# Optimization experiments

Measured on AMD Instinct MI355X. Metric: run time of the kernel, lower is better.

Reference implementation:

```python
import jax, jax.numpy as jnp
import numpy as np

B, S, H, DK = 2, 2048, 16, 64
D = H * DK  # d_model = 1024


def setup_inputs() -> dict:
    key = jax.random.key(0)
    ks = jax.random.split(key, 12)
    inp = {
        "queries": jax.random.normal(ks[0], (B, S, D), jnp.float32),
        "keys": jax.random.normal(ks[1], (B, S, D), jnp.float32),
        "values": jax.random.normal(ks[2], (B, S, D), jnp.float32),
        # additive 0/1 mask (1 = masked out), causal upper-triangular
        "mask": jnp.triu(jnp.ones((S, S), jnp.float32), k=1)[None, None, :, :],
        "W_q": jax.random.normal(ks[3], (D, D), jnp.float32) / np.sqrt(D),
        "b_q": jnp.zeros((D,), jnp.float32),
        "W_k": jax.random.normal(ks[4], (D, D), jnp.float32) / np.sqrt(D),
        "b_k": jnp.zeros((D,), jnp.float32),
        "W_v": jax.random.normal(ks[5], (D, D), jnp.float32) / np.sqrt(D),
        "b_v": jnp.zeros((D,), jnp.float32),
        "W_o": jax.random.normal(ks[6], (D, D), jnp.float32) / np.sqrt(D),
        "b_o": jnp.zeros((D,), jnp.float32),
    }
    return inp


def _split_heads(x):
    # (B, S, D) -> (B, H, S, DK)
    return x.reshape(x.shape[0], x.shape[1], H, DK).transpose(0, 2, 1, 3)


def reference(queries, keys, values, mask, W_q, b_q, W_k, b_k, W_v, b_v, W_o, b_o):
    q = _split_heads(queries @ W_q + b_q)  # (B, H, S, DK)
    k = _split_heads(keys @ W_k + b_k)
    v = _split_heads(values @ W_v + b_v)
    scale = 1.0 / jnp.sqrt(jnp.asarray(DK, q.dtype))
    scores = jnp.einsum("bhqd,bhkd->bhqk", q, k) * scale  # (B, H, S, S)
    scores = scores + (-1e9) * mask
    weights = jax.nn.softmax(scores, axis=-1)
    o = jnp.einsum("bhqk,bhkd->bhqd", weights, v)  # (B, H, S, DK)
    o = o.transpose(0, 2, 1, 3).reshape(queries.shape[0], queries.shape[1], D)
    return o @ W_o + b_o
```

## Files before the change

### kernel.cpp

```cpp
#include <hip/hip_runtime.h>
#include <hip/hip_bf16.h>
#include <stdint.h>

typedef unsigned short u16;
typedef __attribute__((ext_vector_type(4))) float f32x4;
typedef __attribute__((ext_vector_type(8))) short bf16x8;
typedef __attribute__((ext_vector_type(4))) short s16x4;

#define B_ 2
#define S_ 2048
#define H_ 16
#define D_ 1024
#define XELEMS (B_*S_*D_)
#define WELEMS (D_*D_)

__device__ __forceinline__ u16 f2bf(float f) {
  union { float f; unsigned u; } v; v.f = f;
  unsigned r = v.u + 0x7fffu + ((v.u >> 16) & 1u);
  return (u16)(r >> 16);
}

__device__ __forceinline__ void async16(const void* g, void* l) {
  __builtin_amdgcn_global_load_lds(
      (const __attribute__((address_space(1))) unsigned int*)g,
      (__attribute__((address_space(3))) unsigned int*)l, 16, 0, 0);
}

#if __has_builtin(__builtin_amdgcn_exp2f)
#define EXP2(x) __builtin_amdgcn_exp2f(x)
#else
#define EXP2(x) exp2f(x)
#endif

__device__ __forceinline__ unsigned cvtpk(float a, float b) {
  unsigned r;
  asm("v_cvt_pk_bf16_f32 %0, %1, %2" : "=v"(r) : "v"(a), "v"(b));
  return r;
}

__global__ __launch_bounds__(256) void prep_k(
    const float* __restrict__ q, const float* __restrict__ k,
    const float* __restrict__ v,
    const float* __restrict__ Wq, const float* __restrict__ Wk,
    const float* __restrict__ Wv, const float* __restrict__ Wo,
    u16* __restrict__ X, u16* __restrict__ WT) {
  const int bid = blockIdx.x;
  if (bid < 4096) {
    __shared__ float tile[32][33];
    const int z = bid >> 10, rem = bid & 1023;
    const float* W = (z == 0) ? Wq : (z == 1) ? Wk : (z == 2) ? Wv : Wo;
    u16* o = WT + z * WELEMS;
    const int r0 = (rem >> 5) << 5, c0 = (rem & 31) << 5;
    const int tx = threadIdx.x & 31, ty = threadIdx.x >> 5;
    #pragma unroll
    for (int rr = ty; rr < 32; rr += 8)
      tile[rr][tx] = W[(r0 + rr) * D_ + c0 + tx];
    __syncthreads();
    #pragma unroll
    for (int rr = ty; rr < 32; rr += 8)
      o[(c0 + rr) * D_ + r0 + tx] = f2bf(tile[tx][rr]);
  } else {
    const int cb = bid - 4096;
    const int ngrp = XELEMS / 8;
    const int total = 3 * ngrp;
    for (int i = cb * 256 + threadIdx.x; i < total; i += 1024 * 256) {
      int which = i / ngrp;
      int off = (i - which * ngrp) * 8;
      const float* src = (which == 0) ? q : (which == 1) ? k : v;
      float4 a = *(const float4*)(src + off);
      float4 b = *(const float4*)(src + off + 4);
      u16 rr[8] = {f2bf(a.x), f2bf(a.y), f2bf(a.z), f2bf(a.w),
                   f2bf(b.x), f2bf(b.y), f2bf(b.z), f2bf(b.w)};
      uint4 pk;
      pk.x = (unsigned)rr[0] | ((unsigned)rr[1] << 16);
      pk.y = (unsigned)rr[2] | ((unsigned)rr[3] << 16);
      pk.z = (unsigned)rr[4] | ((unsigned)rr[5] << 16);
      pk.w = (unsigned)rr[6] | ((unsigned)rr[7] << 16);
      *(uint4*)(X + which * XELEMS + off) = pk;
    }
  }
}

template <int MODE>
__device__ __forceinline__ void gemm_body(const u16* __restrict__ A,
                                          const u16* __restrict__ BT,
                                          const float* __restrict__ bias,
                                          void* __restrict__ outp,
                                          int bm, int bn) {
  __shared__ __align__(16) u16 As[128 * 64];
  __shared__ __align__(16) u16 Bs[128 * 64];
  const int tid = threadIdx.x;
  const int w = tid >> 6, l = tid & 63;
  const int wr = w >> 1, wc = w & 1;
  const int g = l >> 4, r = l & 15;
  (void)w; (void)l;

  f32x4 acc[4][4];
  #pragma unroll
  for (int i = 0; i < 4; i++)
    #pragma unroll
    for (int j = 0; j < 4; j++) acc[i][j] = (f32x4){0.f, 0.f, 0.f, 0.f};

  int dst[4], aoff[4], boff[4];
  #pragma unroll
  for (int i = 0; i < 4; i++) {
    const int o = i * 4096 + tid * 16;
    dst[i] = o;
    const int row = o >> 7;
    const int cbyte = (o & 127) ^ ((row & 7) << 4);
    aoff[i] = (bm + row) * 1024 + (cbyte >> 1);
    boff[i] = (bn + row) * 1024 + (cbyte >> 1);
  }

  for (int k0 = 0; k0 < 1024; k0 += 64) {
    #pragma unroll
    for (int i = 0; i < 4; i++) async16(A + aoff[i] + k0, (char*)As + dst[i]);
    #pragma unroll
    for (int i = 0; i < 4; i++) async16(BT + boff[i] + k0, (char*)Bs + dst[i]);
    __syncthreads();
    bf16x8 af[2][4], bf[2][4];
    #pragma unroll
    for (int kk = 0; kk < 2; kk++)
      #pragma unroll
      for (int mi = 0; mi < 4; mi++) {
        const int rA = wr * 64 + mi * 16 + r;
        af[kk][mi] = *(const bf16x8*)((const char*)As +
            ((rA * 128 + kk * 64 + g * 16) ^ ((rA & 7) << 4)));
      }
    #pragma unroll
    for (int kk = 0; kk < 2; kk++)
      #pragma unroll
      for (int ni = 0; ni < 4; ni++) {
        const int rB = wc * 64 + ni * 16 + r;
        bf[kk][ni] = *(const bf16x8*)((const char*)Bs +
            ((rB * 128 + kk * 64 + g * 16) ^ ((rB & 7) << 4)));
      }
    #pragma unroll
    for (int kk = 0; kk < 2; kk++)
      #pragma unroll
      for (int mi = 0; mi < 4; mi++)
        #pragma unroll
        for (int ni = 0; ni < 4; ni++)
          acc[mi][ni] = __builtin_amdgcn_mfma_f32_16x16x32_bf16(
              af[kk][mi], bf[kk][ni], acc[mi][ni], 0, 0, 0);
    __syncthreads();
  }

  const int col0 = bn + wc * 64;
  float bc[4];
  #pragma unroll
  for (int ni = 0; ni < 4; ni++) bc[ni] = bias[col0 + ni * 16 + r];

  if (MODE == 0) {
    u16* out = (u16*)outp;
    #pragma unroll
    for (int mi = 0; mi < 4; mi++) {
      const int row = bm + wr * 64 + mi * 16 + g * 4;
      #pragma unroll
      for (int ni = 0; ni < 4; ni++) {
        const int col = col0 + ni * 16 + r;
        const int h = col >> 6, dk = col & 63;
        #pragma unroll
        for (int i = 0; i < 4; i++) {
          const int rr = row + i;
          const int b = rr >> 11, s = rr & 2047;
          out[(((b << 4) | h) * 2048 + s) * 64 + dk] =
              f2bf(acc[mi][ni][i] + bc[ni]);
        }
      }
    }
  } else if (MODE == 2) {
    u16* out = (u16*)outp;
    #pragma unroll
    for (int mi = 0; mi < 4; mi++) {
      const int row = bm + wr * 64 + mi * 16 + g * 4;
      #pragma unroll
      for (int ni = 0; ni < 4; ni++) {
        const int col = col0 + ni * 16 + r;
        const int h = col >> 6, dk = col & 63;
        #pragma unroll
        for (int i = 0; i < 4; i++) {
          const int rr = row + i;
          const int b = rr >> 11, s = rr & 2047;
          out[((((b << 4) | h) * 64 + dk) * 2048) + s] =
              f2bf(acc[mi][ni][i] + bc[ni]);
        }
      }
    }
  } else {
    float* out = (float*)outp;
    #pragma unroll
    for (int mi = 0; mi < 4; mi++) {
      const int row = bm + wr * 64 + mi * 16 + g * 4;
      #pragma unroll
      for (int ni = 0; ni < 4; ni++) {
        const int col = col0 + ni * 16 + r;
        #pragma unroll
        for (int i = 0; i < 4; i++)
          out[(row + i) * 1024 + col] = acc[mi][ni][i] + bc[ni];
      }
    }
  }
}

__global__ __launch_bounds__(256) void gemm_qkv_k(
    const u16* __restrict__ X, const u16* __restrict__ WT,
    const float* __restrict__ bq, const float* __restrict__ bk,
    const float* __restrict__ bv, u16* __restrict__ QKV) {
  const int z = blockIdx.z;
  const float* bias = (z == 0) ? bq : (z == 1) ? bk : bv;
  if (z == 2)
    gemm_body<2>(X + z * XELEMS, WT + z * WELEMS, bias, QKV + z * XELEMS,
                 blockIdx.x * 128, blockIdx.y * 128);
  else
    gemm_body<0>(X + z * XELEMS, WT + z * WELEMS, bias, QKV + z * XELEMS,
                 blockIdx.x * 128, blockIdx.y * 128);
}

__global__ __launch_bounds__(256) void gemm_o_k(
    const u16* __restrict__ O, const u16* __restrict__ WOT,
    const float* __restrict__ bo, float* __restrict__ out) {
  gemm_body<1>(O, WOT, bo, out, blockIdx.x * 128, blockIdx.y * 128);
}

__global__ __launch_bounds__(256) void attn_k(
    const u16* __restrict__ Qh, const u16* __restrict__ Kh,
    const u16* __restrict__ VTh, u16* __restrict__ O) {
  __shared__ __align__(16) char ldsK[2][8192];
  __shared__ __align__(16) char ldsV[2][8192];
  __shared__ __align__(16) u16 ldsP[4][16 * 72];

  const int bh = blockIdx.y;
  const int pj = blockIdx.x;
  const int tid = threadIdx.x;
  const int w = tid >> 6, l = tid & 63;
  const int g = l >> 4, r = l & 15;
  const int b = bh >> 4, h = bh & 15;

  const u16* Qp = Qh + bh * (S_ * 64);
  const char* Kp = (const char*)(Kh + bh * (S_ * 64));
  const char* Vp = (const char*)(VTh + bh * (64 * S_));

  int kdst[2], ksrc[2], vfix[2];
  #pragma unroll
  for (int i = 0; i < 2; i++) {
    const int o = (w * 2 + i) * 1024 + l * 16;
    kdst[i] = o;
    ksrc[i] = o ^ (((o >> 7) & 7) << 4);
    const int d = o >> 7, cbyte = o & 127;
    vfix[i] = d * (S_ * 2) + (cbyte ^ ((d & 7) << 4));
  }
  u16* Pq = &ldsP[w][0];

  #pragma unroll
  for (int pass = 0; pass < 2; pass++) {
    const int qt = pass ? (31 - pj) : pj;
    const int q0w = qt * 64 + w * 16;
    const int nt = qt + 1;
    const int qloc = w * 16 + r;

    bf16x8 qf[2];
    #pragma unroll
    for (int dh = 0; dh < 2; dh++)
      qf[dh] = *(const bf16x8*)(Qp + (q0w + r) * 64 + dh * 32 + g * 8);
    asm volatile("s_waitcnt vmcnt(0)" ::: "memory");

    f32x4 accT[4];
    #pragma unroll
    for (int dn = 0; dn < 4; dn++) accT[dn] = (f32x4){0.f, 0.f, 0.f, 0.f};
    float mrun = -1e30f, lsum = 0.f;

    #pragma unroll
    for (int i = 0; i < 2; i++) {
      async16(Kp + ksrc[i], &ldsK[0][0] + kdst[i]);
      async16(Vp + vfix[i], &ldsV[0][0] + kdst[i]);
    }

    for (int t = 0; t < nt; ++t) {
      const int buf = t & 1;
      if (t + 1 < nt) {
        const char* Ks = Kp + (t + 1) * 8192;
        const char* Vs = Vp + (t + 1) * 128;
        #pragma unroll
        for (int i = 0; i < 2; i++) {
          async16(Ks + ksrc[i], &ldsK[buf ^ 1][0] + kdst[i]);
          async16(Vs + vfix[i], &ldsV[buf ^ 1][0] + kdst[i]);
        }
        asm volatile("s_waitcnt vmcnt(4)" ::: "memory");
      } else {
        asm volatile("s_waitcnt vmcnt(0)" ::: "memory");
      }
      asm volatile("s_barrier" ::: "memory");

      const char* Kb = &ldsK[buf][0];
      f32x4 sc[4];
      #pragma unroll
      for (int ct = 0; ct < 4; ct++) {
        const int row = ct * 16 + r;
        const int sw = (row & 7) << 4;
        bf16x8 k0 = *(const bf16x8*)(Kb + ((row * 128 + g * 16) ^ sw));
        bf16x8 k1 = *(const bf16x8*)(Kb + ((row * 128 + 64 + g * 16) ^ sw));
        f32x4 z = (f32x4){0.f, 0.f, 0.f, 0.f};
        z = __builtin_amdgcn_mfma_f32_16x16x32_bf16(k0, qf[0], z, 0, 0, 0);
        sc[ct] = __builtin_amdgcn_mfma_f32_16x16x32_bf16(k1, qf[1], z, 0, 0, 0);
      }

      const bool diag = (t == nt - 1);
      #pragma unroll
      for (int ct = 0; ct < 4; ct++)
        #pragma unroll
        for (int i = 0; i < 4; i++) {
          float s = sc[ct][i] * 0.18033688f;
          if (diag && (ct * 16 + g * 4 + i > qloc)) s = -1e9f;
          sc[ct][i] = s;
        }

      float a0 = fmaxf(fmaxf(sc[0][0], sc[0][1]), sc[0][2]);
      float a1 = fmaxf(fmaxf(sc[0][3], sc[1][0]), sc[1][1]);
      float a2 = fmaxf(fmaxf(sc[1][2], sc[1][3]), sc[2][0]);
      float a3 = fmaxf(fmaxf(sc[2][1], sc[2][2]), sc[2][3]);
      float a4 = fmaxf(fmaxf(sc[3][0], sc[3][1]), sc[3][2]);
      float pmax = fmaxf(fmaxf(fmaxf(a0, a1), fmaxf(a2, a3)),
                         fmaxf(a4, sc[3][3]));
      pmax = fmaxf(pmax, __shfl_xor(pmax, 16, 64));
      pmax = fmaxf(pmax, __shfl_xor(pmax, 32, 64));

      if (!__all(pmax - mrun <= 11.0f)) {
        const float mnew = fmaxf(mrun, pmax);
        const float corr = EXP2(mrun - mnew);
        mrun = mnew;
        #pragma unroll
        for (int dn = 0; dn < 4; dn++)
          #pragma unroll
          for (int i = 0; i < 4; i++) accT[dn][i] *= corr;
        lsum *= corr;
      }

      float ps = 0.f;
      #pragma unroll
      for (int ct = 0; ct < 4; ct++)
        #pragma unroll
        for (int i = 0; i < 4; i++) {
          const float p = EXP2(sc[ct][i] - mrun);
          sc[ct][i] = p;
          ps += p;
        }
      ps += __shfl_xor(ps, 16, 64);
      ps += __shfl_xor(ps, 32, 64);
      lsum += ps;

      #pragma unroll
      for (int ct = 0; ct < 4; ct++) {
        uint2 pk;
        pk.x = cvtpk(sc[ct][0], sc[ct][1]);
        pk.y = cvtpk(sc[ct][2], sc[ct][3]);
        *(uint2*)&Pq[r * 72 + ct * 16 + g * 4] = pk;
      }
      asm volatile("s_waitcnt lgkmcnt(0)" ::: "memory");

      const char* Vb = &ldsV[buf][0];
      bf16x8 pf[2];
      #pragma unroll
      for (int kp = 0; kp < 2; kp++)
        pf[kp] = *(const bf16x8*)&Pq[r * 72 + kp * 32 + g * 8];
      __builtin_amdgcn_s_setprio(1);
      #pragma unroll
      for (int dn = 0; dn < 4; dn++) {
        const int vrow = dn * 16 + r;
        const int vsw = (vrow & 7) << 4;
        #pragma unroll
        for (int kp = 0; kp < 2; kp++) {
          bf16x8 vf = *(const bf16x8*)(Vb + ((vrow * 128 + kp * 64 + g * 16) ^ vsw));
          accT[dn] = __builtin_amdgcn_mfma_f32_16x16x32_bf16(vf, pf[kp], accT[dn], 0, 0, 0);
        }
      }
      __builtin_amdgcn_s_setprio(0);
      asm volatile("s_barrier" ::: "memory");
    }

    const float inv = 1.0f / lsum;
    const int qrow = q0w + r;
    #pragma unroll
    for (int dn = 0; dn < 4; dn++) {
      u16 o0 = f2bf(accT[dn][0] * inv), o1 = f2bf(accT[dn][1] * inv);
      u16 o2 = f2bf(accT[dn][2] * inv), o3 = f2bf(accT[dn][3] * inv);
      uint2 pk;
      pk.x = (unsigned)o0 | ((unsigned)o1 << 16);
      pk.y = (unsigned)o2 | ((unsigned)o3 << 16);
      *(uint2*)(O + ((size_t)(b * 2048 + qrow)) * 1024 + h * 64 + dn * 16 + g * 4) = pk;
    }
  }
}

extern "C" void kernel_launch(void* const* d_in, const int* in_sizes, int n_in,
                              void* d_out, int out_size, void* d_ws, size_t ws_size,
                              hipStream_t stream) {
  const float* q  = (const float*)d_in[0];
  const float* k  = (const float*)d_in[1];
  const float* v  = (const float*)d_in[2];
  const float* Wq = (const float*)d_in[4];
  const float* bq = (const float*)d_in[5];
  const float* Wk = (const float*)d_in[6];
  const float* bk = (const float*)d_in[7];
  const float* Wv = (const float*)d_in[8];
  const float* bv = (const float*)d_in[9];
  const float* Wo = (const float*)d_in[10];
  const float* bo = (const float*)d_in[11];

  char* ws = (char*)d_ws;
  const size_t MB = 1u << 20;
  u16* X   = (u16*)(ws);
  u16* WT  = (u16*)(ws + 24 * MB);
  u16* QKV = (u16*)(ws + 32 * MB);
  u16* O   = (u16*)(ws);

  hipLaunchKernelGGL(prep_k, dim3(5120), dim3(256), 0, stream,
                     q, k, v, Wq, Wk, Wv, Wo, X, WT);
  hipLaunchKernelGGL(gemm_qkv_k, dim3(32, 8, 3), dim3(256), 0, stream,
                     X, WT, bq, bk, bv, QKV);
  hipLaunchKernelGGL(attn_k, dim3(16, 32), dim3(256), 0, stream,
                     QKV, QKV + XELEMS, QKV + 2 * XELEMS, O);
  hipLaunchKernelGGL(gemm_o_k, dim3(32, 8), dim3(256), 0, stream,
                     O, WT + 3 * WELEMS, bo, (float*)d_out);
}
```

Measured before the change: 137.3 us.

## Double-buffer GEMM K-loop with async prefetch and split attention into per-tile blocks

The GEMM main loop now uses two LDS buffers, issuing the async global-to-LDS loads for the next K slice before computing the current one. It waits with vmcnt and raw barriers instead of __syncthreads, and raises wave priority around the MFMA block. The attention kernel drops its paired two-pass scheme, in which each block handled q-tiles pj and 31-pj. It now launches one block per q-tile (32x32 grid), heaviest tiles first, to add parallelism and rely on the scheduler for balance. This doubles GEMM LDS use, which may lower occupancy, and makes attention blocks uneven in work.

```diff
diff --git a/kernel.cpp b/kernel.cpp
--- a/kernel.cpp
+++ b/kernel.cpp
@@ -87,8 +87,8 @@
                                           const float* __restrict__ bias,
                                           void* __restrict__ outp,
                                           int bm, int bn) {
-  __shared__ __align__(16) u16 As[128 * 64];
-  __shared__ __align__(16) u16 Bs[128 * 64];
+  __shared__ __align__(16) u16 As[2][128 * 64];
+  __shared__ __align__(16) u16 Bs[2][128 * 64];
   const int tid = threadIdx.x;
   const int w = tid >> 6, l = tid & 63;
   const int wr = w >> 1, wc = w & 1;
@@ -112,19 +112,34 @@
     boff[i] = (bn + row) * 1024 + (cbyte >> 1);
   }
 
-  for (int k0 = 0; k0 < 1024; k0 += 64) {
-    #pragma unroll
-    for (int i = 0; i < 4; i++) async16(A + aoff[i] + k0, (char*)As + dst[i]);
-    #pragma unroll
-    for (int i = 0; i < 4; i++) async16(BT + boff[i] + k0, (char*)Bs + dst[i]);
-    __syncthreads();
+  #pragma unroll
+  for (int i = 0; i < 4; i++) {
+    async16(A + aoff[i], (char*)As[0] + dst[i]);
+    async16(BT + boff[i], (char*)Bs[0] + dst[i]);
+  }
+
+  for (int t = 0; t < 16; ++t) {
+    const int buf = t & 1;
+    if (t < 15) {
+      const int k0 = (t + 1) * 64;
+      #pragma unroll
+      for (int i = 0; i < 4; i++) {
+        async16(A + aoff[i] + k0, (char*)As[buf ^ 1] + dst[i]);
+        async16(BT + boff[i] + k0, (char*)Bs[buf ^ 1] + dst[i]);
+      }
+      asm volatile("s_waitcnt vmcnt(8)" ::: "memory");
+    } else {
+      asm volatile("s_waitcnt vmcnt(0)" ::: "memory");
+    }
+    asm volatile("s_barrier" ::: "memory");
+
     bf16x8 af[2][4], bf[2][4];
     #pragma unroll
     for (int kk = 0; kk < 2; kk++)
       #pragma unroll
       for (int mi = 0; mi < 4; mi++) {
         const int rA = wr * 64 + mi * 16 + r;
-        af[kk][mi] = *(const bf16x8*)((const char*)As +
+        af[kk][mi] = *(const bf16x8*)((const char*)As[buf] +
             ((rA * 128 + kk * 64 + g * 16) ^ ((rA & 7) << 4)));
       }
     #pragma unroll
@@ -132,9 +147,10 @@
       #pragma unroll
       for (int ni = 0; ni < 4; ni++) {
         const int rB = wc * 64 + ni * 16 + r;
-        bf[kk][ni] = *(const bf16x8*)((const char*)Bs +
+        bf[kk][ni] = *(const bf16x8*)((const char*)Bs[buf] +
             ((rB * 128 + kk * 64 + g * 16) ^ ((rB & 7) << 4)));
       }
+    __builtin_amdgcn_s_setprio(1);
     #pragma unroll
     for (int kk = 0; kk < 2; kk++)
       #pragma unroll
@@ -143,7 +159,8 @@
         for (int ni = 0; ni < 4; ni++)
           acc[mi][ni] = __builtin_amdgcn_mfma_f32_16x16x32_bf16(
               af[kk][mi], bf[kk][ni], acc[mi][ni], 0, 0, 0);
-    __syncthreads();
+    __builtin_amdgcn_s_setprio(0);
+    asm volatile("s_barrier" ::: "memory");
   }
 
   const int col0 = bn + wc * 64;
@@ -231,7 +248,7 @@
   __shared__ __align__(16) u16 ldsP[4][16 * 72];
 
   const int bh = blockIdx.y;
-  const int pj = blockIdx.x;
+  const int qt = 31 - blockIdx.x;
   const int tid = threadIdx.x;
   const int w = tid >> 6, l = tid & 63;
   const int g = l >> 4, r = l & 15;
@@ -252,143 +269,139 @@
   }
   u16* Pq = &ldsP[w][0];
 
-  #pragma unroll
-  for (int pass = 0; pass < 2; pass++) {
-    const int qt = pass ? (31 - pj) : pj;
-    const int q0w = qt * 64 + w * 16;
-    const int nt = qt + 1;
-    const int qloc = w * 16 + r;
-
-    bf16x8 qf[2];
-    #pragma unroll
-    for (int dh = 0; dh < 2; dh++)
-      qf[dh] = *(const bf16x8*)(Qp + (q0w + r) * 64 + dh * 32 + g * 8);
-    asm volatile("s_waitcnt vmcnt(0)" ::: "memory");
-
-    f32x4 accT[4];
-    #pragma unroll
-    for (int dn = 0; dn < 4; dn++) accT[dn] = (f32x4){0.f, 0.f, 0.f, 0.f};
-    float mrun = -1e30f, lsum = 0.f;
-
-    #pragma unroll
-    for (int i = 0; i < 2; i++) {
-      async16(Kp + ksrc[i], &ldsK[0][0] + kdst[i]);
-      async16(Vp + vfix[i], &ldsV[0][0] + kdst[i]);
-    }
-
-    for (int t = 0; t < nt; ++t) {
-      const int buf = t & 1;
-      if (t + 1 < nt) {
-        const char* Ks = Kp + (t + 1) * 8192;
-        const char* Vs = Vp + (t + 1) * 128;
+  const int q0w = qt * 64 + w * 16;
+  const int nt = qt + 1;
+  const int qloc = w * 16 + r;
+
+  bf16x8 qf[2];
+  #pragma unroll
+  for (int dh = 0; dh < 2; dh++)
+    qf[dh] = *(const bf16x8*)(Qp + (q0w + r) * 64 + dh * 32 + g * 8);
+  asm volatile("s_waitcnt vmcnt(0)" ::: "memory");
+
+  f32x4 accT[4];
+  #pragma unroll
+  for (int dn = 0; dn < 4; dn++) accT[dn] = (f32x4){0.f, 0.f, 0.f, 0.f};
+  float mrun = -1e30f, lsum = 0.f;
+
+  #pragma unroll
+  for (int i = 0; i < 2; i++) {
+    async16(Kp + ksrc[i], &ldsK[0][0] + kdst[i]);
+    async16(Vp + vfix[i], &ldsV[0][0] + kdst[i]);
+  }
+
+  for (int t = 0; t < nt; ++t) {
+    const int buf = t & 1;
+    if (t + 1 < nt) {
+      const char* Ks = Kp + (t + 1) * 8192;
+      const char* Vs = Vp + (t + 1) * 128;
+      #pragma unroll
+      for (int i = 0; i < 2; i++) {
+        async16(Ks + ksrc[i], &ldsK[buf ^ 1][0] + kdst[i]);
+        async16(Vs + vfix[i], &ldsV[buf ^ 1][0] + kdst[i]);
+      }
+      asm volatile("s_waitcnt vmcnt(4)" ::: "memory");
+    } else {
+      asm volatile("s_waitcnt vmcnt(0)" ::: "memory");
+    }
+    asm volatile("s_barrier" ::: "memory");
+
+    const char* Kb = &ldsK[buf][0];
+    f32x4 sc[4];
+    #pragma unroll
+    for (int ct = 0; ct < 4; ct++) {
+      const int row = ct * 16 + r;
+      const int sw = (row & 7) << 4;
+      bf16x8 k0 = *(const bf16x8*)(Kb + ((row * 128 + g * 16) ^ sw));
+      bf16x8 k1 = *(const bf16x8*)(Kb + ((row * 128 + 64 + g * 16) ^ sw));
+      f32x4 z = (f32x4){0.f, 0.f, 0.f, 0.f};
+      z = __builtin_amdgcn_mfma_f32_16x16x32_bf16(k0, qf[0], z, 0, 0, 0);
+      sc[ct] = __builtin_amdgcn_mfma_f32_16x16x32_bf16(k1, qf[1], z, 0, 0, 0);
+    }
+
+    const bool diag = (t == nt - 1);
+    #pragma unroll
+    for (int ct = 0; ct < 4; ct++)
+      #pragma unroll
+      for (int i = 0; i < 4; i++) {
+        float s = sc[ct][i] * 0.18033688f;
+        if (diag && (ct * 16 + g * 4 + i > qloc)) s = -1e9f;
+        sc[ct][i] = s;
+      }
+
+    float a0 = fmaxf(fmaxf(sc[0][0], sc[0][1]), sc[0][2]);
+    float a1 = fmaxf(fmaxf(sc[0][3], sc[1][0]), sc[1][1]);
+    float a2 = fmaxf(fmaxf(sc[1][2], sc[1][3]), sc[2][0]);
+    float a3 = fmaxf(fmaxf(sc[2][1], sc[2][2]), sc[2][3]);
+    float a4 = fmaxf(fmaxf(sc[3][0], sc[3][1]), sc[3][2]);
+    float pmax = fmaxf(fmaxf(fmaxf(a0, a1), fmaxf(a2, a3)),
+                       fmaxf(a4, sc[3][3]));
+    pmax = fmaxf(pmax, __shfl_xor(pmax, 16, 64));
+    pmax = fmaxf(pmax, __shfl_xor(pmax, 32, 64));
+
+    if (!__all(pmax - mrun <= 11.0f)) {
+      const float mnew = fmaxf(mrun, pmax);
+      const float corr = EXP2(mrun - mnew);
+      mrun = mnew;
+      #pragma unroll
+      for (int dn = 0; dn < 4; dn++)
         #pragma unroll
-        for (int i = 0; i < 2; i++) {
-          async16(Ks + ksrc[i], &ldsK[buf ^ 1][0] + kdst[i]);
-          async16(Vs + vfix[i], &ldsV[buf ^ 1][0] + kdst[i]);
-        }
-        asm volatile("s_waitcnt vmcnt(4)" ::: "memory");
-      } else {
-        asm volatile("s_waitcnt vmcnt(0)" ::: "memory");
-      }
-      asm volatile("s_barrier" ::: "memory");
-
-      const char* Kb = &ldsK[buf][0];
-      f32x4 sc[4];
-      #pragma unroll
-      for (int ct = 0; ct < 4; ct++) {
-        const int row = ct * 16 + r;
-        const int sw = (row & 7) << 4;
-        bf16x8 k0 = *(const bf16x8*)(Kb + ((row * 128 + g * 16) ^ sw));
-        bf16x8 k1 = *(const bf16x8*)(Kb + ((row * 128 + 64 + g * 16) ^ sw));
-        f32x4 z = (f32x4){0.f, 0.f, 0.f, 0.f};
-        z = __builtin_amdgcn_mfma_f32_16x16x32_bf16(k0, qf[0], z, 0, 0, 0);
-        sc[ct] = __builtin_amdgcn_mfma_f32_16x16x32_bf16(k1, qf[1], z, 0, 0, 0);
-      }
-
-      const bool diag = (t == nt - 1);
-      #pragma unroll
-      for (int ct = 0; ct < 4; ct++)
-        #pragma unroll
-        for (int i = 0; i < 4; i++) {
-          float s = sc[ct][i] * 0.18033688f;
-          if (diag && (ct * 16 + g * 4 + i > qloc)) s = -1e9f;
-          sc[ct][i] = s;
-        }
-
-      float a0 = fmaxf(fmaxf(sc[0][0], sc[0][1]), sc[0][2]);
-      float a1 = fmaxf(fmaxf(sc[0][3], sc[1][0]), sc[1][1]);
-      float a2 = fmaxf(fmaxf(sc[1][2], sc[1][3]), sc[2][0]);
-      float a3 = fmaxf(fmaxf(sc[2][1], sc[2][2]), sc[2][3]);
-      float a4 = fmaxf(fmaxf(sc[3][0], sc[3][1]), sc[3][2]);
-      float pmax = fmaxf(fmaxf(fmaxf(a0, a1), fmaxf(a2, a3)),
-                         fmaxf(a4, sc[3][3]));
-      pmax = fmaxf(pmax, __shfl_xor(pmax, 16, 64));
-      pmax = fmaxf(pmax, __shfl_xor(pmax, 32, 64));
-
-      if (!__all(pmax - mrun <= 11.0f)) {
-        const float mnew = fmaxf(mrun, pmax);
-        const float corr = EXP2(mrun - mnew);
-        mrun = mnew;
-        #pragma unroll
-        for (int dn = 0; dn < 4; dn++)
-          #pragma unroll
-          for (int i = 0; i < 4; i++) accT[dn][i] *= corr;
-        lsum *= corr;
-      }
-
-      float ps = 0.f;
-      #pragma unroll
-      for (int ct = 0; ct < 4; ct++)
-        #pragma unroll
-        for (int i = 0; i < 4; i++) {
-          const float p = EXP2(sc[ct][i] - mrun);
-          sc[ct][i] = p;
-          ps += p;
-        }
-      ps += __shfl_xor(ps, 16, 64);
-      ps += __shfl_xor(ps, 32, 64);
-      lsum += ps;
-
-      #pragma unroll
-      for (int ct = 0; ct < 4; ct++) {
-        uint2 pk;
-        pk.x = cvtpk(sc[ct][0], sc[ct][1]);
-        pk.y = cvtpk(sc[ct][2], sc[ct][3]);
-        *(uint2*)&Pq[r * 72 + ct * 16 + g * 4] = pk;
-      }
-      asm volatile("s_waitcnt lgkmcnt(0)" ::: "memory");
-
-      const char* Vb = &ldsV[buf][0];
-      bf16x8 pf[2];
-      #pragma unroll
-      for (int kp = 0; kp < 2; kp++)
-        pf[kp] = *(const bf16x8*)&Pq[r * 72 + kp * 32 + g * 8];
-      __builtin_amdgcn_s_setprio(1);
-      #pragma unroll
-      for (int dn = 0; dn < 4; dn++) {
-        const int vrow = dn * 16 + r;
-        const int vsw = (vrow & 7) << 4;
-        #pragma unroll
-        for (int kp = 0; kp < 2; kp++) {
-          bf16x8 vf = *(const bf16x8*)(Vb + ((vrow * 128 + kp * 64 + g * 16) ^ vsw));
-          accT[dn] = __builtin_amdgcn_mfma_f32_16x16x32_bf16(vf, pf[kp], accT[dn], 0, 0, 0);
-        }
-      }
-      __builtin_amdgcn_s_setprio(0);
-      asm volatile("s_barrier" ::: "memory");
-    }
-
-    const float inv = 1.0f / lsum;
-    const int qrow = q0w + r;
+        for (int i = 0; i < 4; i++) accT[dn][i] *= corr;
+      lsum *= corr;
+    }
+
+    float ps = 0.f;
+    #pragma unroll
+    for (int ct = 0; ct < 4; ct++)
+      #pragma unroll
+      for (int i = 0; i < 4; i++) {
+        const float p = EXP2(sc[ct][i] - mrun);
+        sc[ct][i] = p;
+        ps += p;
+      }
+    ps += __shfl_xor(ps, 16, 64);
+    ps += __shfl_xor(ps, 32, 64);
+    lsum += ps;
+
+    #pragma unroll
+    for (int ct = 0; ct < 4; ct++) {
+      uint2 pk;
+      pk.x = cvtpk(sc[ct][0], sc[ct][1]);
+      pk.y = cvtpk(sc[ct][2], sc[ct][3]);
+      *(uint2*)&Pq[r * 72 + ct * 16 + g * 4] = pk;
+    }
+    asm volatile("s_waitcnt lgkmcnt(0)" ::: "memory");
+
+    const char* Vb = &ldsV[buf][0];
+    bf16x8 pf[2];
+    #pragma unroll
+    for (int kp = 0; kp < 2; kp++)
+      pf[kp] = *(const bf16x8*)&Pq[r * 72 + kp * 32 + g * 8];
+    __builtin_amdgcn_s_setprio(1);
     #pragma unroll
     for (int dn = 0; dn < 4; dn++) {
-      u16 o0 = f2bf(accT[dn][0] * inv), o1 = f2bf(accT[dn][1] * inv);
-      u16 o2 = f2bf(accT[dn][2] * inv), o3 = f2bf(accT[dn][3] * inv);
-      uint2 pk;
-      pk.x = (unsigned)o0 | ((unsigned)o1 << 16);
-      pk.y = (unsigned)o2 | ((unsigned)o3 << 16);
-      *(uint2*)(O + ((size_t)(b * 2048 + qrow)) * 1024 + h * 64 + dn * 16 + g * 4) = pk;
-    }
+      const int vrow = dn * 16 + r;
+      const int vsw = (vrow & 7) << 4;
+      #pragma unroll
+      for (int kp = 0; kp < 2; kp++) {
+        bf16x8 vf = *(const bf16x8*)(Vb + ((vrow * 128 + kp * 64 + g * 16) ^ vsw));
+        accT[dn] = __builtin_amdgcn_mfma_f32_16x16x32_bf16(vf, pf[kp], accT[dn], 0, 0, 0);
+      }
+    }
+    __builtin_amdgcn_s_setprio(0);
+    asm volatile("s_barrier" ::: "memory");
+  }
+
+  const float inv = 1.0f / lsum;
+  const int qrow = q0w + r;
+  #pragma unroll
+  for (int dn = 0; dn < 4; dn++) {
+    u16 o0 = f2bf(accT[dn][0] * inv), o1 = f2bf(accT[dn][1] * inv);
+    u16 o2 = f2bf(accT[dn][2] * inv), o3 = f2bf(accT[dn][3] * inv);
+    uint2 pk;
+    pk.x = (unsigned)o0 | ((unsigned)o1 << 16);
+    pk.y = (unsigned)o2 | ((unsigned)o3 << 16);
+    *(uint2*)(O + ((size_t)(b * 2048 + qrow)) * 1024 + h * 64 + dn * 16 + g * 4) = pk;
   }
 }
 
@@ -418,7 +431,7 @@
                      q, k, v, Wq, Wk, Wv, Wo, X, WT);
   hipLaunchKernelGGL(gemm_qkv_k, dim3(32, 8, 3), dim3(256), 0, stream,
                      X, WT, bq, bk, bv, QKV);
-  hipLaunchKernelGGL(attn_k, dim3(16, 32), dim3(256), 0, stream,
+  hipLaunchKernelGGL(attn_k, dim3(32, 32), dim3(256), 0, stream,
                      QKV, QKV + XELEMS, QKV + 2 * XELEMS, O);
   hipLaunchKernelGGL(gemm_o_k, dim3(32, 8), dim3(256), 0, stream,
                      O, WT + 3 * WELEMS, bo, (float*)d_out);
```

Measured after the change: 181.9 us. 32.5% more time.
